# Kernel optimization log

Measured on AMD Instinct MI355X. Metric: run time of the kernel, lower is better.

The kernel has to match this reference:

```python
import jax, jax.numpy as jnp
import numpy as np

D_MODEL, D_Q, D_K, D_V, N = 1024, 128, 128, 128, 8192

def setup_inputs() -> dict:
    key = jax.random.key(0)
    ks = jax.random.split(key, 7)
    s = 1.0 / np.sqrt(D_MODEL)
    return {
        "x": jax.random.normal(ks[0], (N, D_MODEL), dtype=jnp.float32),
        "Wq": jax.random.uniform(ks[1], (D_MODEL, D_Q), jnp.float32, -s, s),
        "bq": jax.random.uniform(ks[2], (D_Q,), jnp.float32, -s, s),
        "Wk": jax.random.uniform(ks[3], (D_MODEL, D_K), jnp.float32, -s, s),
        "bk": jax.random.uniform(ks[4], (D_K,), jnp.float32, -s, s),
        "Wv": jax.random.uniform(ks[5], (D_MODEL, D_V), jnp.float32, -s, s),
        "bv": jax.random.uniform(ks[6], (D_V,), jnp.float32, -s, s),
    }

def reference(x, Wq, bq, Wk, bk, Wv, bv):
    q = x @ Wq + bq          # [N, d_q]
    k = x @ Wk + bk          # [N, d_k]
    v = x @ Wv + bv          # [N, d_v]
    scale = jnp.sqrt(jnp.asarray(q.shape[-1], q.dtype))
    scores = (q @ k.T) / scale          # [N, N]
    attn = jax.nn.softmax(scores, axis=1)  # matches nn.Softmax(dim=1) on 2D
    return attn @ v                     # [N, d_v]
```

## Files before the change

kernel.cpp:

```cpp
#include <hip/hip_runtime.h>


typedef __attribute__((ext_vector_type(8))) short bf16x8;
typedef __attribute__((ext_vector_type(4))) float f32x4;

#define NTOK 8192
#define DMODEL 1024
#define DH 128
#define NSPLIT 8
#define CPS 32

__device__ __forceinline__ unsigned short f2bf(float f) {
  unsigned int u = __builtin_bit_cast(unsigned int, f);
  u += 0x7fffu + ((u >> 16) & 1u);
  return (unsigned short)(u >> 16);
}

__device__ __forceinline__ unsigned int pack2bf(float a, float b) {
  return (unsigned int)f2bf(a) | ((unsigned int)f2bf(b) << 16);
}

__device__ __forceinline__ void gl2lds16(const void* gp, void* lp) {
  const __attribute__((address_space(1))) unsigned int* g =
      (const __attribute__((address_space(1))) unsigned int*)gp;
  __attribute__((address_space(3))) unsigned int* l =
      (__attribute__((address_space(3))) unsigned int*)lp;
  __builtin_amdgcn_global_load_lds(g, l, 16, 0, 0);
}

__global__ __launch_bounds__(256) void k_build_wt(const float* __restrict__ Wq,
                                                  const float* __restrict__ Wk,
                                                  const float* __restrict__ Wv,
                                                  unsigned short* __restrict__ wt) {
  __shared__ unsigned short tile[32 * 130];
  int k0 = blockIdx.x * 32;
  int p = blockIdx.y;
  int t = threadIdx.x;
  const float* W = (p == 0) ? Wq : ((p == 1) ? Wk : Wv);
  float vscale = (p == 2) ? 0.0625f : 1.0f;
#pragma unroll
  for (int i = 0; i < 16; i++) {
    int e = i * 256 + t;
    int n = e & 127, kk = e >> 7;
    tile[kk * 130 + n] = f2bf(W[(size_t)(k0 + kk) * DH + n] * vscale);
  }
  __syncthreads();
#pragma unroll
  for (int i = 0; i < 16; i++) {
    int e = i * 256 + t;
    int kk = e & 31, n = e >> 5;
    wt[(size_t)(p * DH + n) * DMODEL + k0 + kk] = tile[kk * 130 + n];
  }
}

__global__ __launch_bounds__(256, 2) void k_qkv(const float* __restrict__ x,
                                                const unsigned short* __restrict__ wt,
                                                const float* __restrict__ bq,
                                                const float* __restrict__ bk,
                                                const float* __restrict__ bv,
                                                unsigned short* __restrict__ qs,
                                                unsigned short* __restrict__ kkv,
                                                unsigned short* __restrict__ vt) {
  __shared__ float xt[2][64 * 64];
  __shared__ unsigned short wtt[2][128 * 64];
  int mt = blockIdx.x, p = blockIdx.y;
  int tid = threadIdx.x;
  int w = tid >> 6, lane = tid & 63, l16 = lane & 15, g = lane >> 4;

#define STAGE_QKV(buf, k0)                                                     \
  {                                                                            \
    _Pragma("unroll") for (int r = 0; r < 4; r++) {                            \
      int seg = r * 4 + w;                                                     \
      int xr = seg * 4 + (lane >> 4);                                          \
      int xlc = ((lane & 15) ^ (xr & 15)) & 15;                                \
      gl2lds16(&x[(size_t)(mt * 64 + xr) * DMODEL + (k0) + xlc * 4],           \
               &xt[buf][seg * 256]);                                           \
      int wc = seg * 8 + (lane >> 3);                                          \
      int wlc = ((lane & 7) ^ (wc & 7)) & 7;                                   \
      gl2lds16(&wt[(size_t)(p * DH + wc) * DMODEL + (k0) + wlc * 8],           \
               &wtt[buf][seg * 512]);                                          \
    }                                                                          \
  }

  f32x4 zero = {0.f, 0.f, 0.f, 0.f};
  f32x4 acc[8];
#pragma unroll
  for (int i = 0; i < 8; i++) acc[i] = zero;

  STAGE_QKV(0, 0);
  int arow = w * 16 + l16;
  for (int kt2 = 0; kt2 < 16; kt2++) {
    int b = kt2 & 1;
    __syncthreads();
    if (kt2 < 15) STAGE_QKV(b ^ 1, (kt2 + 1) * 64);

    bf16x8 a[2];
#pragma unroll
    for (int half = 0; half < 2; half++) {
      int lc0 = half * 8 + g * 2;
      const f32x4 u0 = *(const f32x4*)&xt[b][arow * 64 + ((lc0 ^ l16) & 15) * 4];
      const f32x4 u1 = *(const f32x4*)&xt[b][arow * 64 + (((lc0 + 1) ^ l16) & 15) * 4];
      union { unsigned int u[4]; bf16x8 v; } pk;
      pk.u[0] = pack2bf(u0[0], u0[1]);
      pk.u[1] = pack2bf(u0[2], u0[3]);
      pk.u[2] = pack2bf(u1[0], u1[1]);
      pk.u[3] = pack2bf(u1[2], u1[3]);
      a[half] = pk.v;
    }
#pragma unroll
    for (int nt = 0; nt < 8; nt++) {
      int col = nt * 16 + l16;
#pragma unroll
      for (int half = 0; half < 2; half++) {
        int lc = half * 4 + g;
        bf16x8 bf = *(const bf16x8*)&wtt[b][col * 64 + ((lc ^ (col & 7)) & 7) * 8];
        acc[nt] = __builtin_amdgcn_mfma_f32_16x16x32_bf16(a[half], bf, acc[nt], 0, 0, 0);
      }
    }
  }
#undef STAGE_QKV

  const float* bias = (p == 0) ? bq : ((p == 1) ? bk : bv);
  float mult = (p == 0) ? (0.08838834764831845f * 1.44269504088896340f) : 1.0f;
  if (p < 2) {
    unsigned short* outp = (p == 0) ? qs : kkv;
#pragma unroll
    for (int nt = 0; nt < 8; nt++) {
      int col = nt * 16 + l16;
      float bsv = bias[col];
#pragma unroll
      for (int r = 0; r < 4; r++) {
        int row = mt * 64 + w * 16 + g * 4 + r;
        outp[(size_t)row * DH + col] = f2bf((acc[nt][r] + bsv) * mult);
      }
    }
  } else {
#pragma unroll
    for (int nt = 0; nt < 8; nt++) {
      int col = nt * 16 + l16;
      float bsv = bias[col] * 0.0625f;
      int row0 = mt * 64 + w * 16 + g * 4;
      uint2 uv;
      uv.x = pack2bf(acc[nt][0] + bsv, acc[nt][1] + bsv);
      uv.y = pack2bf(acc[nt][2] + bsv, acc[nt][3] + bsv);
      *(uint2*)(&vt[(size_t)col * NTOK + row0]) = uv;
    }
  }
}

__global__ __launch_bounds__(128, 2) void k_flash(const unsigned short* __restrict__ qs,
                                                  const unsigned short* __restrict__ kkv,
                                                  const unsigned short* __restrict__ vt,
                                                  _Float16* __restrict__ opart,
                                                  float* __restrict__ lpart) {
  __shared__ unsigned short kt[2][32 * 128];
  __shared__ unsigned short vtl[2][128 * 32];
  __shared__ unsigned short pscr[2 * 2 * 512];
  int sp = blockIdx.x, qt = blockIdx.y;
  int tid = threadIdx.x;
  int w = tid >> 6, lane = tid & 63, l16 = lane & 15, g = lane >> 4;
  int sw4 = (l16 >> 1) & 3;

  bf16x8 qf[2][4];
  int qbase = qt * 64 + w * 32;
#pragma unroll
  for (int q2 = 0; q2 < 2; q2++)
#pragma unroll
    for (int f = 0; f < 4; f++)
      qf[q2][f] = *(const bf16x8*)(&qs[(size_t)(qbase + q2 * 16 + l16) * DH + f * 32 + g * 8]);

  int pcK[4];
#pragma unroll
  for (int f = 0; f < 4; f++) {
    int lc = f * 4 + g;
    pcK[f] = (lc & 8) | ((lc ^ l16) & 7);
  }
  int pcP = (g ^ sw4) & 3;

#define STAGE_FLASH(buf, chunk)                                                  \
  {                                                                              \
    int key0 = (chunk) * 32;                                                     \
    _Pragma("unroll") for (int ii = 0; ii < 4; ii++) {                           \
      int i = w * 4 + ii;                                                        \
      int krow = 4 * i + (lane >> 4);                                            \
      int klc = ((lane & 15) & 8) | (((lane & 15) ^ krow) & 7);                  \
      gl2lds16(&kkv[(size_t)(key0 + krow) * DH + klc * 8], &kt[buf][i * 512]);   \
      int vrow = 16 * i + (lane >> 2);                                           \
      gl2lds16(&vt[(size_t)vrow * NTOK + key0 + (lane & 3) * 8],                 \
               &vtl[buf][i * 512]);                                              \
    }                                                                            \
  }

  f32x4 zero = {0.f, 0.f, 0.f, 0.f};
  f32x4 o[2][8];
#pragma unroll
  for (int q2 = 0; q2 < 2; q2++)
#pragma unroll
    for (int dt = 0; dt < 8; dt++) o[q2][dt] = zero;
  float l[2] = {0.f, 0.f};

  int c0 = sp * CPS;
  STAGE_FLASH(0, c0);

  for (int it = 0; it < CPS; it++) {
    int b = it & 1;
    __syncthreads();
    if (it + 1 < CPS) STAGE_FLASH(b ^ 1, c0 + it + 1);

    f32x4 s[2][2];
#pragma unroll
    for (int q2 = 0; q2 < 2; q2++)
#pragma unroll
      for (int mt = 0; mt < 2; mt++) s[q2][mt] = zero;
    __builtin_amdgcn_s_setprio(1);
#pragma unroll
    for (int mt = 0; mt < 2; mt++) {
      bf16x8 kf[4];
#pragma unroll
      for (int f = 0; f < 4; f++)
        kf[f] = *(const bf16x8*)(&kt[b][(mt * 16 + l16) * 128 + pcK[f] * 8]);
#pragma unroll
      for (int f = 0; f < 4; f++) {
        s[0][mt] = __builtin_amdgcn_mfma_f32_16x16x32_bf16(kf[f], qf[0][f], s[0][mt], 0, 0, 0);
        s[1][mt] = __builtin_amdgcn_mfma_f32_16x16x32_bf16(kf[f], qf[1][f], s[1][mt], 0, 0, 0);
      }
    }
    __builtin_amdgcn_s_setprio(0);

#pragma unroll
    for (int q2 = 0; q2 < 2; q2++) {
      unsigned short* pw = &pscr[(w * 2 + q2) * 512];
      float ssum = 0.f;
#pragma unroll
      for (int mt = 0; mt < 2; mt++) {
        float p0 = __builtin_amdgcn_exp2f(s[q2][mt][0]);
        float p1 = __builtin_amdgcn_exp2f(s[q2][mt][1]);
        float p2 = __builtin_amdgcn_exp2f(s[q2][mt][2]);
        float p3 = __builtin_amdgcn_exp2f(s[q2][mt][3]);
        ssum += (p0 + p1) + (p2 + p3);
        uint2 uv;
        uv.x = pack2bf(p0, p1);
        uv.y = pack2bf(p2, p3);
        int ch = ((mt * 2 + (g >> 1)) ^ sw4) & 3;
        *(uint2*)(&pw[l16 * 32 + ch * 8 + (g & 1) * 4]) = uv;
      }
      l[q2] += ssum;
    }

    bf16x8 pb[2];
#pragma unroll
    for (int q2 = 0; q2 < 2; q2++)
      pb[q2] = *(const bf16x8*)(&pscr[(w * 2 + q2) * 512 + l16 * 32 + pcP * 8]);

    __builtin_amdgcn_s_setprio(1);
#pragma unroll
    for (int dt = 0; dt < 8; dt++) {
      bf16x8 vf = *(const bf16x8*)(&vtl[b][(dt * 16 + l16) * 32 + g * 8]);
      o[0][dt] = __builtin_amdgcn_mfma_f32_16x16x32_bf16(vf, pb[0], o[0][dt], 0, 0, 0);
      o[1][dt] = __builtin_amdgcn_mfma_f32_16x16x32_bf16(vf, pb[1], o[1][dt], 0, 0, 0);
    }
    __builtin_amdgcn_s_setprio(0);
  }
#undef STAGE_FLASH

#pragma unroll
  for (int q2 = 0; q2 < 2; q2++) {
    l[q2] += __shfl_xor(l[q2], 16);
    l[q2] += __shfl_xor(l[q2], 32);
    int qrow = qbase + q2 * 16 + l16;
    size_t obase = ((size_t)sp * NTOK + qrow) * DH;
#pragma unroll
    for (int dt = 0; dt < 8; dt++) {
      union { _Float16 h[4]; uint2 u; } pk;
      pk.h[0] = (_Float16)o[q2][dt][0];
      pk.h[1] = (_Float16)o[q2][dt][1];
      pk.h[2] = (_Float16)o[q2][dt][2];
      pk.h[3] = (_Float16)o[q2][dt][3];
      *(uint2*)(&opart[obase + dt * 16 + g * 4]) = pk.u;
    }
    if (g == 0) lpart[sp * NTOK + qrow] = l[q2];
  }
}

__global__ __launch_bounds__(256) void k_merge(const _Float16* __restrict__ opart,
                                               const float* __restrict__ lpart,
                                               float* __restrict__ out) {
  int gid = blockIdx.x * 256 + threadIdx.x;
  int row = gid >> 6, cp = gid & 63;
  float den = 0.f, n0 = 0.f, n1 = 0.f;
#pragma unroll
  for (int s = 0; s < NSPLIT; s++) {
    den += lpart[s * NTOK + row];
    union { unsigned int u; _Float16 h[2]; } v;
    v.u = *(const unsigned int*)&opart[((size_t)s * NTOK + row) * DH + cp * 2];
    n0 += (float)v.h[0];
    n1 += (float)v.h[1];
  }
  float inv = 16.0f / den;
  *(float2*)&out[(size_t)row * DH + cp * 2] = make_float2(n0 * inv, n1 * inv);
}

extern "C" void kernel_launch(void* const* d_in, const int* in_sizes, int n_in,
                              void* d_out, int out_size, void* d_ws, size_t ws_size,
                              hipStream_t stream) {
  const float* x  = (const float*)d_in[0];
  const float* Wq = (const float*)d_in[1];
  const float* bq = (const float*)d_in[2];
  const float* Wk = (const float*)d_in[3];
  const float* bk = (const float*)d_in[4];
  const float* Wv = (const float*)d_in[5];
  const float* bv = (const float*)d_in[6];
  float* out = (float*)d_out;

  char* ws = (char*)d_ws;
  _Float16*       opart = (_Float16*)(ws);
  unsigned short* wt  = (unsigned short*)(ws + 16777216);
  unsigned short* qsb = (unsigned short*)(ws + 17563648);
  unsigned short* kkb = (unsigned short*)(ws + 19660800);
  unsigned short* vtb = (unsigned short*)(ws + 21757952);
  float* lpart = (float*)(ws + 23855104);

  k_build_wt<<<dim3(32, 3), 256, 0, stream>>>(Wq, Wk, Wv, wt);
  k_qkv<<<dim3(128, 3), 256, 0, stream>>>(x, wt, bq, bk, bv, qsb, kkb, vtb);
  k_flash<<<dim3(NSPLIT, 128), 128, 0, stream>>>(qsb, kkb, vtb, opart, lpart);
  k_merge<<<2048, 256, 0, stream>>>(opart, lpart, out);
}
```

Measured before the change: 158.8 us.

## Widen flash blocks to 8 waves splitting keys across wave pairs with LDS reduction

```diff
diff --git a/kernel.cpp b/kernel.cpp
--- a/kernel.cpp
+++ b/kernel.cpp
@@ -8,7 +8,7 @@
 #define DMODEL 1024
 #define DH 128
 #define NSPLIT 8
-#define CPS 32
+#define CPS 16
 
 __device__ __forceinline__ unsigned short f2bf(float f) {
   unsigned int u = __builtin_bit_cast(unsigned int, f);
@@ -148,21 +148,23 @@
   }
 }
 
-__global__ __launch_bounds__(128, 2) void k_flash(const unsigned short* __restrict__ qs,
+__global__ __launch_bounds__(512, 4) void k_flash(const unsigned short* __restrict__ qs,
                                                   const unsigned short* __restrict__ kkv,
                                                   const unsigned short* __restrict__ vt,
                                                   _Float16* __restrict__ opart,
                                                   float* __restrict__ lpart) {
-  __shared__ unsigned short kt[2][32 * 128];
-  __shared__ unsigned short vtl[2][128 * 32];
-  __shared__ unsigned short pscr[2 * 2 * 512];
+  __shared__ unsigned short smem[40960];
+  unsigned short* kt = smem;
+  unsigned short* vtl = smem + 16384;
+  unsigned short* pscr = smem + 32768;
   int sp = blockIdx.x, qt = blockIdx.y;
   int tid = threadIdx.x;
   int w = tid >> 6, lane = tid & 63, l16 = lane & 15, g = lane >> 4;
+  int kg = w & 1, qg = w >> 1;
   int sw4 = (l16 >> 1) & 3;
 
   bf16x8 qf[2][4];
-  int qbase = qt * 64 + w * 32;
+  int qbase = qt * 128 + qg * 32;
 #pragma unroll
   for (int q2 = 0; q2 < 2; q2++)
 #pragma unroll
@@ -175,19 +177,22 @@
     int lc = f * 4 + g;
     pcK[f] = (lc & 8) | ((lc ^ l16) & 7);
   }
+  int pcV = ((kg * 4 + g) ^ l16) & 7;
   int pcP = (g ^ sw4) & 3;
 
 #define STAGE_FLASH(buf, chunk)                                                  \
   {                                                                              \
-    int key0 = (chunk) * 32;                                                     \
-    _Pragma("unroll") for (int ii = 0; ii < 4; ii++) {                           \
-      int i = w * 4 + ii;                                                        \
+    int key0 = (chunk) * 64;                                                     \
+    _Pragma("unroll") for (int ii = 0; ii < 2; ii++) {                           \
+      int i = w * 2 + ii;                                                        \
       int krow = 4 * i + (lane >> 4);                                            \
       int klc = ((lane & 15) & 8) | (((lane & 15) ^ krow) & 7);                  \
-      gl2lds16(&kkv[(size_t)(key0 + krow) * DH + klc * 8], &kt[buf][i * 512]);   \
-      int vrow = 16 * i + (lane >> 2);                                           \
-      gl2lds16(&vt[(size_t)vrow * NTOK + key0 + (lane & 3) * 8],                 \
-               &vtl[buf][i * 512]);                                              \
+      gl2lds16(&kkv[(size_t)(key0 + krow) * DH + klc * 8],                       \
+               &kt[(buf)*8192 + i * 512]);                                       \
+      int vrow = 8 * i + (lane >> 3);                                            \
+      int vlc = ((lane & 7) ^ vrow) & 7;                                         \
+      gl2lds16(&vt[(size_t)vrow * NTOK + key0 + vlc * 8],                        \
+               &vtl[(buf)*8192 + i * 512]);                                      \
     }                                                                            \
   }
 
@@ -218,7 +223,7 @@
       bf16x8 kf[4];
 #pragma unroll
       for (int f = 0; f < 4; f++)
-        kf[f] = *(const bf16x8*)(&kt[b][(mt * 16 + l16) * 128 + pcK[f] * 8]);
+        kf[f] = *(const bf16x8*)(&kt[b * 8192 + (kg * 32 + mt * 16 + l16) * 128 + pcK[f] * 8]);
 #pragma unroll
       for (int f = 0; f < 4; f++) {
         s[0][mt] = __builtin_amdgcn_mfma_f32_16x16x32_bf16(kf[f], qf[0][f], s[0][mt], 0, 0, 0);
@@ -255,7 +260,7 @@
     __builtin_amdgcn_s_setprio(1);
 #pragma unroll
     for (int dt = 0; dt < 8; dt++) {
-      bf16x8 vf = *(const bf16x8*)(&vtl[b][(dt * 16 + l16) * 32 + g * 8]);
+      bf16x8 vf = *(const bf16x8*)(&vtl[b * 8192 + (dt * 16 + l16) * 64 + pcV * 8]);
       o[0][dt] = __builtin_amdgcn_mfma_f32_16x16x32_bf16(vf, pb[0], o[0][dt], 0, 0, 0);
       o[1][dt] = __builtin_amdgcn_mfma_f32_16x16x32_bf16(vf, pb[1], o[1][dt], 0, 0, 0);
     }
@@ -263,22 +268,39 @@
   }
 #undef STAGE_FLASH
 
-#pragma unroll
-  for (int q2 = 0; q2 < 2; q2++) {
-    l[q2] += __shfl_xor(l[q2], 16);
-    l[q2] += __shfl_xor(l[q2], 32);
-    int qrow = qbase + q2 * 16 + l16;
-    size_t obase = ((size_t)sp * NTOK + qrow) * DH;
-#pragma unroll
-    for (int dt = 0; dt < 8; dt++) {
-      union { _Float16 h[4]; uint2 u; } pk;
-      pk.h[0] = (_Float16)o[q2][dt][0];
-      pk.h[1] = (_Float16)o[q2][dt][1];
-      pk.h[2] = (_Float16)o[q2][dt][2];
-      pk.h[3] = (_Float16)o[q2][dt][3];
-      *(uint2*)(&opart[obase + dt * 16 + g * 4]) = pk.u;
-    }
-    if (g == 0) lpart[sp * NTOK + qrow] = l[q2];
+  __syncthreads();
+  float* osc = (float*)smem;
+  float* lsc = (float*)pscr;
+  if (kg == 1) {
+#pragma unroll
+    for (int q2 = 0; q2 < 2; q2++) {
+#pragma unroll
+      for (int dt = 0; dt < 8; dt++)
+        *(f32x4*)&osc[(((qg * 2 + q2) * 8 + dt) << 8) + lane * 4] = o[q2][dt];
+      lsc[(qg * 2 + q2) * 64 + lane] = l[q2];
+    }
+  }
+  __syncthreads();
+  if (kg == 0) {
+#pragma unroll
+    for (int q2 = 0; q2 < 2; q2++) {
+      l[q2] += lsc[(qg * 2 + q2) * 64 + lane];
+      l[q2] += __shfl_xor(l[q2], 16);
+      l[q2] += __shfl_xor(l[q2], 32);
+      int qrow = qbase + q2 * 16 + l16;
+      size_t obase = ((size_t)sp * NTOK + qrow) * DH;
+#pragma unroll
+      for (int dt = 0; dt < 8; dt++) {
+        f32x4 t = *(const f32x4*)&osc[(((qg * 2 + q2) * 8 + dt) << 8) + lane * 4];
+        union { _Float16 h[4]; uint2 u; } pk;
+        pk.h[0] = (_Float16)(o[q2][dt][0] + t[0]);
+        pk.h[1] = (_Float16)(o[q2][dt][1] + t[1]);
+        pk.h[2] = (_Float16)(o[q2][dt][2] + t[2]);
+        pk.h[3] = (_Float16)(o[q2][dt][3] + t[3]);
+        *(uint2*)(&opart[obase + dt * 16 + g * 4]) = pk.u;
+      }
+      if (g == 0) lpart[sp * NTOK + qrow] = l[q2];
+    }
   }
 }
 
@@ -322,6 +344,6 @@
 
   k_build_wt<<<dim3(32, 3), 256, 0, stream>>>(Wq, Wk, Wv, wt);
   k_qkv<<<dim3(128, 3), 256, 0, stream>>>(x, wt, bq, bk, bv, qsb, kkb, vtb);
-  k_flash<<<dim3(NSPLIT, 128), 128, 0, stream>>>(qsb, kkb, vtb, opart, lpart);
+  k_flash<<<dim3(NSPLIT, 64), 512, 0, stream>>>(qsb, kkb, vtb, opart, lpart);
   k_merge<<<2048, 256, 0, stream>>>(opart, lpart, out);
 }
```

New measurement: 189.8 us. 1.2x slower.
